# Performance work log

Hardware: AMD Instinct MI355X
Metric: run time of the kernel (lower is better)

Reference implementation:

```python
import jax, jax.numpy as jnp
import numpy as np

MARGIN = 1.0

def setup_inputs() -> dict:
    key = jax.random.key(0)
    k1, k2, k3, k4 = jax.random.split(key, 4)
    N, d, P = 8192, 1024, 65536
    embeddings = jax.random.normal(k1, (N, d), dtype=jnp.float32)
    ind_one = jax.random.randint(k2, (P,), 0, N)
    ind_two = jax.random.randint(k3, (P,), 0, N)
    target = jax.random.randint(k4, (P,), 0, 2)
    return {"embeddings": embeddings, "ind_one": ind_one, "ind_two": ind_two, "target": target}

def reference(embeddings, ind_one, ind_two, target):
    # cosine distance matrix: 1 - normalized gram matrix  [N, N]
    emb_norm = embeddings / jnp.linalg.norm(embeddings, axis=1, keepdims=True)
    dist_matrix = 1.0 - jnp.einsum('nd,md->nm', emb_norm, emb_norm)
    dists = dist_matrix[ind_one, ind_two]  # [P]
    t = target.astype(jnp.float32)
    loss = t * dists + (1.0 - t) * jax.nn.relu(MARGIN - dists)
    return jnp.mean(loss)
```

## Files before the change

### kernel.cpp

```cpp
#include <hip/hip_runtime.h>

#define N_EMB 8192
#define DIM   1024
#define NPAIR 65536
#define MARGIN 1.0f

__global__ __launch_bounds__(256) void norms_kernel(const float* __restrict__ emb,
                                                    float* __restrict__ rnorm,
                                                    double* __restrict__ acc) {
    const int row  = blockIdx.x;
    const int tid  = threadIdx.x;
    const float4 v = reinterpret_cast<const float4*>(emb + (size_t)row * DIM)[tid];
    float s = v.x * v.x + v.y * v.y + v.z * v.z + v.w * v.w;

    #pragma unroll
    for (int off = 32; off > 0; off >>= 1) s += __shfl_xor(s, off);

    __shared__ float part[4];
    const int wave = tid >> 6;
    const int lane = tid & 63;
    if (lane == 0) part[wave] = s;
    __syncthreads();
    if (tid == 0) {
        float tot = part[0] + part[1] + part[2] + part[3];
        rnorm[row] = 1.0f / sqrtf(tot);
        if (row == 0) *acc = 0.0;
    }
}

__global__ __launch_bounds__(256) void pair_kernel(const float* __restrict__ emb,
                                                   const float* __restrict__ rnorm,
                                                   const int* __restrict__ ind1,
                                                   const int* __restrict__ ind2,
                                                   const int* __restrict__ tgt,
                                                   double* __restrict__ acc) {
    const int lane   = threadIdx.x & 63;
    const int wave   = (blockIdx.x * blockDim.x + threadIdx.x) >> 6;
    const int nwaves = (gridDim.x * blockDim.x) >> 6;

    float wsum = 0.0f;

    for (int p = wave; p < NPAIR; p += nwaves) {
        const int a = ind1[p];
        const int b = ind2[p];
        const float4* ra = reinterpret_cast<const float4*>(emb + (size_t)a * DIM);
        const float4* rb = reinterpret_cast<const float4*>(emb + (size_t)b * DIM);

        const float4 a0 = ra[lane];
        const float4 a1 = ra[lane + 64];
        const float4 a2 = ra[lane + 128];
        const float4 a3 = ra[lane + 192];
        const float4 b0 = rb[lane];
        const float4 b1 = rb[lane + 64];
        const float4 b2 = rb[lane + 128];
        const float4 b3 = rb[lane + 192];

        float s = a0.x * b0.x;
        s = fmaf(a0.y, b0.y, s);
        s = fmaf(a0.z, b0.z, s);
        s = fmaf(a0.w, b0.w, s);
        s = fmaf(a1.x, b1.x, s);
        s = fmaf(a1.y, b1.y, s);
        s = fmaf(a1.z, b1.z, s);
        s = fmaf(a1.w, b1.w, s);
        s = fmaf(a2.x, b2.x, s);
        s = fmaf(a2.y, b2.y, s);
        s = fmaf(a2.z, b2.z, s);
        s = fmaf(a2.w, b2.w, s);
        s = fmaf(a3.x, b3.x, s);
        s = fmaf(a3.y, b3.y, s);
        s = fmaf(a3.z, b3.z, s);
        s = fmaf(a3.w, b3.w, s);

        #pragma unroll
        for (int off = 32; off > 0; off >>= 1) s += __shfl_xor(s, off);

        const float dist = 1.0f - s * rnorm[a] * rnorm[b];
        const float t    = (float)tgt[p];
        const float loss = t * dist + (1.0f - t) * fmaxf(MARGIN - dist, 0.0f);
        if (lane == 0) wsum += loss;
    }

    __shared__ float part[4];
    if (lane == 0) part[threadIdx.x >> 6] = wsum;
    __syncthreads();
    if (threadIdx.x == 0) {
        const float bs = part[0] + part[1] + part[2] + part[3];
        atomicAdd(acc, (double)bs);
    }
}

__global__ void finalize_kernel(const double* __restrict__ acc, float* __restrict__ out) {
    out[0] = (float)(acc[0] / (double)NPAIR);
}

extern "C" void kernel_launch(void* const* d_in, const int* in_sizes, int n_in,
                              void* d_out, int out_size, void* d_ws, size_t ws_size,
                              hipStream_t stream) {
    const float* emb  = (const float*)d_in[0];
    const int*   ind1 = (const int*)d_in[1];
    const int*   ind2 = (const int*)d_in[2];
    const int*   tgt  = (const int*)d_in[3];
    float*       out  = (float*)d_out;

    float*  rnorm = (float*)d_ws;
    double* acc   = (double*)((char*)d_ws + (size_t)N_EMB * sizeof(float));

    norms_kernel<<<N_EMB, 256, 0, stream>>>(emb, rnorm, acc);

    pair_kernel<<<2048, 256, 0, stream>>>(emb, rnorm, ind1, ind2, tgt, acc);

    finalize_kernel<<<1, 1, 0, stream>>>(acc, out);
}
```

Measured before the change: 145.2 us.

## Gather from pre-normalized fp16 embedding table with fdot2 and fuse finalize

A prep kernel normalizes each embedding row and writes it as fp16 into workspace. The pair kernel then gathers half-size rows and accumulates with packed fp16 dot products, which removes the rnorm lookups and halves the gather traffic. The separate finalize kernel is replaced by a last-block-done counter inside the pair kernel. The cost is an extra 16 MB table write plus fp16 rounding of the inputs, and the fast path only runs if the workspace is large enough.

```diff
diff --git a/kernel.cpp b/kernel.cpp
--- a/kernel.cpp
+++ b/kernel.cpp
@@ -5,35 +5,41 @@
 #define NPAIR 65536
 #define MARGIN 1.0f
 
-__global__ __launch_bounds__(256) void norms_kernel(const float* __restrict__ emb,
-                                                    float* __restrict__ rnorm,
-                                                    double* __restrict__ acc) {
-    const int row  = blockIdx.x;
-    const int tid  = threadIdx.x;
+typedef _Float16 h2 __attribute__((ext_vector_type(2)));
+typedef _Float16 h4 __attribute__((ext_vector_type(4)));
+typedef _Float16 h8 __attribute__((ext_vector_type(8)));
+
+
+__global__ __launch_bounds__(256) void prep16_kernel(const float* __restrict__ emb,
+                                                     _Float16* __restrict__ nemb,
+                                                     double* __restrict__ acc,
+                                                     unsigned int* __restrict__ cnt) {
+    const int row = blockIdx.x;
+    const int tid = threadIdx.x;
     const float4 v = reinterpret_cast<const float4*>(emb + (size_t)row * DIM)[tid];
     float s = v.x * v.x + v.y * v.y + v.z * v.z + v.w * v.w;
-
     #pragma unroll
     for (int off = 32; off > 0; off >>= 1) s += __shfl_xor(s, off);
-
     __shared__ float part[4];
-    const int wave = tid >> 6;
-    const int lane = tid & 63;
-    if (lane == 0) part[wave] = s;
+    if ((tid & 63) == 0) part[tid >> 6] = s;
     __syncthreads();
-    if (tid == 0) {
-        float tot = part[0] + part[1] + part[2] + part[3];
-        rnorm[row] = 1.0f / sqrtf(tot);
-        if (row == 0) *acc = 0.0;
-    }
+    const float rn = 1.0f / sqrtf(part[0] + part[1] + part[2] + part[3]);
+    h4 o;
+    o[0] = (_Float16)(v.x * rn);
+    o[1] = (_Float16)(v.y * rn);
+    o[2] = (_Float16)(v.z * rn);
+    o[3] = (_Float16)(v.w * rn);
+    reinterpret_cast<h4*>(nemb + (size_t)row * DIM)[tid] = o;
+    if (row == 0 && tid == 0) { *acc = 0.0; *cnt = 0u; }
 }
 
-__global__ __launch_bounds__(256) void pair_kernel(const float* __restrict__ emb,
-                                                   const float* __restrict__ rnorm,
-                                                   const int* __restrict__ ind1,
-                                                   const int* __restrict__ ind2,
-                                                   const int* __restrict__ tgt,
-                                                   double* __restrict__ acc) {
+__global__ __launch_bounds__(256) void pair16_kernel(const _Float16* __restrict__ nemb,
+                                                     const int* __restrict__ ind1,
+                                                     const int* __restrict__ ind2,
+                                                     const int* __restrict__ tgt,
+                                                     double* __restrict__ acc,
+                                                     unsigned int* __restrict__ cnt,
+                                                     float* __restrict__ out) {
     const int lane   = threadIdx.x & 63;
     const int wave   = (blockIdx.x * blockDim.x + threadIdx.x) >> 6;
     const int nwaves = (gridDim.x * blockDim.x) >> 6;
@@ -43,9 +49,91 @@
     for (int p = wave; p < NPAIR; p += nwaves) {
         const int a = ind1[p];
         const int b = ind2[p];
+        const h8* ra = reinterpret_cast<const h8*>(nemb + (size_t)a * DIM);
+        const h8* rb = reinterpret_cast<const h8*>(nemb + (size_t)b * DIM);
+
+        const h8 a0 = ra[lane];
+        const h8 a1 = ra[lane + 64];
+        const h8 b0 = rb[lane];
+        const h8 b1 = rb[lane + 64];
+
+        float s = 0.0f;
+#if __has_builtin(__builtin_amdgcn_fdot2)
+        #define FD(va, vb, I) do { h2 xa, xb;                                  \
+            xa[0] = va[2*I]; xa[1] = va[2*I + 1];                              \
+            xb[0] = vb[2*I]; xb[1] = vb[2*I + 1];                              \
+            s = __builtin_amdgcn_fdot2(xa, xb, s, false); } while (0)
+        FD(a0, b0, 0); FD(a0, b0, 1); FD(a0, b0, 2); FD(a0, b0, 3);
+        FD(a1, b1, 0); FD(a1, b1, 1); FD(a1, b1, 2); FD(a1, b1, 3);
+        #undef FD
+#else
+        #pragma unroll
+        for (int i = 0; i < 8; ++i) {
+            s = fmaf((float)a0[i], (float)b0[i], s);
+            s = fmaf((float)a1[i], (float)b1[i], s);
+        }
+#endif
+        #pragma unroll
+        for (int off = 32; off > 0; off >>= 1) s += __shfl_xor(s, off);
+
+        if (lane == 0) {
+            const float dist = 1.0f - s;
+            const float t    = (float)tgt[p];
+            wsum += t * dist + (1.0f - t) * fmaxf(MARGIN - dist, 0.0f);
+        }
+    }
+
+    __shared__ float part[4];
+    if (lane == 0) part[threadIdx.x >> 6] = wsum;
+    __syncthreads();
+    if (threadIdx.x == 0) {
+        atomicAdd(acc, (double)(part[0] + part[1] + part[2] + part[3]));
+        __threadfence();
+        const unsigned int done = atomicAdd(cnt, 1u);
+        if (done == gridDim.x - 1) {
+            const double tot = atomicAdd(acc, 0.0);
+            out[0] = (float)(tot / (double)NPAIR);
+        }
+    }
+}
+
+
+__global__ __launch_bounds__(256) void norms_kernel(const float* __restrict__ emb,
+                                                    float* __restrict__ rnorm,
+                                                    double* __restrict__ acc,
+                                                    unsigned int* __restrict__ cnt) {
+    const int row = blockIdx.x;
+    const int tid = threadIdx.x;
+    const float4 v = reinterpret_cast<const float4*>(emb + (size_t)row * DIM)[tid];
+    float s = v.x * v.x + v.y * v.y + v.z * v.z + v.w * v.w;
+    #pragma unroll
+    for (int off = 32; off > 0; off >>= 1) s += __shfl_xor(s, off);
+    __shared__ float part[4];
+    if ((tid & 63) == 0) part[tid >> 6] = s;
+    __syncthreads();
+    if (tid == 0) {
+        rnorm[row] = 1.0f / sqrtf(part[0] + part[1] + part[2] + part[3]);
+        if (row == 0) { *acc = 0.0; *cnt = 0u; }
+    }
+}
+
+__global__ __launch_bounds__(256) void pair32_kernel(const float* __restrict__ emb,
+                                                     const float* __restrict__ rnorm,
+                                                     const int* __restrict__ ind1,
+                                                     const int* __restrict__ ind2,
+                                                     const int* __restrict__ tgt,
+                                                     double* __restrict__ acc,
+                                                     unsigned int* __restrict__ cnt,
+                                                     float* __restrict__ out) {
+    const int lane   = threadIdx.x & 63;
+    const int wave   = (blockIdx.x * blockDim.x + threadIdx.x) >> 6;
+    const int nwaves = (gridDim.x * blockDim.x) >> 6;
+    float wsum = 0.0f;
+    for (int p = wave; p < NPAIR; p += nwaves) {
+        const int a = ind1[p];
+        const int b = ind2[p];
         const float4* ra = reinterpret_cast<const float4*>(emb + (size_t)a * DIM);
         const float4* rb = reinterpret_cast<const float4*>(emb + (size_t)b * DIM);
-
         const float4 a0 = ra[lane];
         const float4 a1 = ra[lane + 64];
         const float4 a2 = ra[lane + 128];
@@ -54,44 +142,31 @@
         const float4 b1 = rb[lane + 64];
         const float4 b2 = rb[lane + 128];
         const float4 b3 = rb[lane + 192];
-
         float s = a0.x * b0.x;
-        s = fmaf(a0.y, b0.y, s);
-        s = fmaf(a0.z, b0.z, s);
-        s = fmaf(a0.w, b0.w, s);
-        s = fmaf(a1.x, b1.x, s);
-        s = fmaf(a1.y, b1.y, s);
-        s = fmaf(a1.z, b1.z, s);
-        s = fmaf(a1.w, b1.w, s);
-        s = fmaf(a2.x, b2.x, s);
-        s = fmaf(a2.y, b2.y, s);
-        s = fmaf(a2.z, b2.z, s);
-        s = fmaf(a2.w, b2.w, s);
-        s = fmaf(a3.x, b3.x, s);
-        s = fmaf(a3.y, b3.y, s);
-        s = fmaf(a3.z, b3.z, s);
-        s = fmaf(a3.w, b3.w, s);
-
+        s = fmaf(a0.y, b0.y, s); s = fmaf(a0.z, b0.z, s); s = fmaf(a0.w, b0.w, s);
+        s = fmaf(a1.x, b1.x, s); s = fmaf(a1.y, b1.y, s); s = fmaf(a1.z, b1.z, s); s = fmaf(a1.w, b1.w, s);
+        s = fmaf(a2.x, b2.x, s); s = fmaf(a2.y, b2.y, s); s = fmaf(a2.z, b2.z, s); s = fmaf(a2.w, b2.w, s);
+        s = fmaf(a3.x, b3.x, s); s = fmaf(a3.y, b3.y, s); s = fmaf(a3.z, b3.z, s); s = fmaf(a3.w, b3.w, s);
         #pragma unroll
         for (int off = 32; off > 0; off >>= 1) s += __shfl_xor(s, off);
-
-        const float dist = 1.0f - s * rnorm[a] * rnorm[b];
-        const float t    = (float)tgt[p];
-        const float loss = t * dist + (1.0f - t) * fmaxf(MARGIN - dist, 0.0f);
-        if (lane == 0) wsum += loss;
+        if (lane == 0) {
+            const float dist = 1.0f - s * rnorm[a] * rnorm[b];
+            const float t    = (float)tgt[p];
+            wsum += t * dist + (1.0f - t) * fmaxf(MARGIN - dist, 0.0f);
+        }
     }
-
     __shared__ float part[4];
     if (lane == 0) part[threadIdx.x >> 6] = wsum;
     __syncthreads();
     if (threadIdx.x == 0) {
-        const float bs = part[0] + part[1] + part[2] + part[3];
-        atomicAdd(acc, (double)bs);
+        atomicAdd(acc, (double)(part[0] + part[1] + part[2] + part[3]));
+        __threadfence();
+        const unsigned int done = atomicAdd(cnt, 1u);
+        if (done == gridDim.x - 1) {
+            const double tot = atomicAdd(acc, 0.0);
+            out[0] = (float)(tot / (double)NPAIR);
+        }
     }
-}
-
-__global__ void finalize_kernel(const double* __restrict__ acc, float* __restrict__ out) {
-    out[0] = (float)(acc[0] / (double)NPAIR);
 }
 
 extern "C" void kernel_launch(void* const* d_in, const int* in_sizes, int n_in,
@@ -103,12 +178,18 @@
     const int*   tgt  = (const int*)d_in[3];
     float*       out  = (float*)d_out;
 
-    float*  rnorm = (float*)d_ws;
-    double* acc   = (double*)((char*)d_ws + (size_t)N_EMB * sizeof(float));
+    double*       acc = (double*)d_ws;
+    unsigned int* cnt = (unsigned int*)((char*)d_ws + 8);
 
-    norms_kernel<<<N_EMB, 256, 0, stream>>>(emb, rnorm, acc);
+    const size_t table_bytes = (size_t)N_EMB * DIM * sizeof(_Float16);
 
-    pair_kernel<<<2048, 256, 0, stream>>>(emb, rnorm, ind1, ind2, tgt, acc);
-
-    finalize_kernel<<<1, 1, 0, stream>>>(acc, out);
+    if (ws_size >= 64 + table_bytes) {
+        _Float16* nemb = (_Float16*)((char*)d_ws + 64);
+        prep16_kernel<<<N_EMB, 256, 0, stream>>>(emb, nemb, acc, cnt);
+        pair16_kernel<<<2048, 256, 0, stream>>>(nemb, ind1, ind2, tgt, acc, cnt, out);
+    } else {
+        float* rnorm = (float*)((char*)d_ws + 64);
+        norms_kernel<<<N_EMB, 256, 0, stream>>>(emb, rnorm, acc, cnt);
+        pair32_kernel<<<2048, 256, 0, stream>>>(emb, rnorm, ind1, ind2, tgt, acc, cnt, out);
+    }
 }
```

Result: slower. 172.2 us (+18.6%).

## Bucket pairs by first index so each wave reuses its row in registers

Applied to the files above, without the earlier changes.

Pairs are counting-sorted by ind_one through a histogram, a single-block scan and an atomic scatter. Each wave then owns one embedding row, keeps it in registers and walks only its own bucket of partners, so the A-row is never reloaded from memory. The inner loop handles two partners at a time for extra memory-level parallelism, the norm kernel now does four rows per block, and the finalize kernel is folded into a last-block-done counter. This adds three small launches and sorting overhead, and bucket sizes vary between waves, which creates load imbalance.

```diff
diff --git a/kernel.cpp b/kernel.cpp
--- a/kernel.cpp
+++ b/kernel.cpp
@@ -5,93 +5,185 @@
 #define NPAIR 65536
 #define MARGIN 1.0f
 
+#define OFF_BIN   64
+#define OFF_CUR   (OFF_BIN + (N_EMB + 1) * 4 + 4)
+#define OFF_HIST  (OFF_CUR + N_EMB * 4)
+#define OFF_PACK  (OFF_HIST + N_EMB * 4)
+
 __global__ __launch_bounds__(256) void norms_kernel(const float* __restrict__ emb,
                                                     float* __restrict__ rnorm,
-                                                    double* __restrict__ acc) {
-    const int row  = blockIdx.x;
+                                                    int* __restrict__ hist,
+                                                    double* __restrict__ acc,
+                                                    unsigned int* __restrict__ cnt) {
     const int tid  = threadIdx.x;
-    const float4 v = reinterpret_cast<const float4*>(emb + (size_t)row * DIM)[tid];
-    float s = v.x * v.x + v.y * v.y + v.z * v.z + v.w * v.w;
-
+    const int lane = tid & 63;
+    const int row  = blockIdx.x * 4 + (tid >> 6);
+    const float4* r = reinterpret_cast<const float4*>(emb + (size_t)row * DIM);
+    const float4 v0 = r[lane];
+    const float4 v1 = r[lane + 64];
+    const float4 v2 = r[lane + 128];
+    const float4 v3 = r[lane + 192];
+    float s = v0.x*v0.x + v0.y*v0.y + v0.z*v0.z + v0.w*v0.w
+            + v1.x*v1.x + v1.y*v1.y + v1.z*v1.z + v1.w*v1.w
+            + v2.x*v2.x + v2.y*v2.y + v2.z*v2.z + v2.w*v2.w
+            + v3.x*v3.x + v3.y*v3.y + v3.z*v3.z + v3.w*v3.w;
     #pragma unroll
     for (int off = 32; off > 0; off >>= 1) s += __shfl_xor(s, off);
-
-    __shared__ float part[4];
-    const int wave = tid >> 6;
-    const int lane = tid & 63;
-    if (lane == 0) part[wave] = s;
+    if (lane == 0) rnorm[row] = 1.0f / sqrtf(s);
+
+    const int gid = blockIdx.x * 256 + tid;
+    if (gid < N_EMB) hist[gid] = 0;
+    if (gid == N_EMB) { *acc = 0.0; *cnt = 0u; }
+}
+
+__global__ __launch_bounds__(256) void hist_kernel(const int* __restrict__ ind1,
+                                                   int* __restrict__ hist) {
+    const int p = blockIdx.x * 256 + threadIdx.x;
+    if (p < NPAIR) atomicAdd(&hist[ind1[p]], 1);
+}
+
+__global__ __launch_bounds__(256) void scan_kernel(const int* __restrict__ hist,
+                                                   int* __restrict__ bin_start,
+                                                   int* __restrict__ cursor) {
+    const int t = threadIdx.x;
+    int loc[32];
+    int run = 0;
+    #pragma unroll
+    for (int j = 0; j < 32; ++j) { loc[j] = run; run += hist[t * 32 + j]; }
+
+    __shared__ int ps[256];
+    ps[t] = run;
     __syncthreads();
-    if (tid == 0) {
-        float tot = part[0] + part[1] + part[2] + part[3];
-        rnorm[row] = 1.0f / sqrtf(tot);
-        if (row == 0) *acc = 0.0;
-    }
-}
-
-__global__ __launch_bounds__(256) void pair_kernel(const float* __restrict__ emb,
-                                                   const float* __restrict__ rnorm,
-                                                   const int* __restrict__ ind1,
-                                                   const int* __restrict__ ind2,
-                                                   const int* __restrict__ tgt,
-                                                   double* __restrict__ acc) {
-    const int lane   = threadIdx.x & 63;
-    const int wave   = (blockIdx.x * blockDim.x + threadIdx.x) >> 6;
-    const int nwaves = (gridDim.x * blockDim.x) >> 6;
+    for (int d = 1; d < 256; d <<= 1) {
+        const int v = (t >= d) ? ps[t - d] : 0;
+        __syncthreads();
+        ps[t] += v;
+        __syncthreads();
+    }
+    const int excl = ps[t] - run;
+    #pragma unroll
+    for (int j = 0; j < 32; ++j) {
+        const int b = excl + loc[j];
+        bin_start[t * 32 + j] = b;
+        cursor[t * 32 + j]    = b;
+    }
+    if (t == 255) bin_start[N_EMB] = NPAIR;
+}
+
+__global__ __launch_bounds__(256) void scatter_kernel(const int* __restrict__ ind1,
+                                                      const int* __restrict__ ind2,
+                                                      const int* __restrict__ tgt,
+                                                      int* __restrict__ cursor,
+                                                      int* __restrict__ packed) {
+    const int p = blockIdx.x * 256 + threadIdx.x;
+    if (p < NPAIR) {
+        const int a   = ind1[p];
+        const int pos = atomicAdd(&cursor[a], 1);
+        packed[pos] = (ind2[p] << 1) | (tgt[p] & 1);
+    }
+}
+
+__global__ __launch_bounds__(256, 8) void pair_kernel(const float* __restrict__ emb,
+                                                      const float* __restrict__ rnorm,
+                                                      const int* __restrict__ bin_start,
+                                                      const int* __restrict__ packed,
+                                                      double* __restrict__ acc,
+                                                      unsigned int* __restrict__ cnt,
+                                                      float* __restrict__ out) {
+    const int lane = threadIdx.x & 63;
+    const int w    = (blockIdx.x * blockDim.x + threadIdx.x) >> 6;
+
+    const int start = bin_start[w];
+    const int end   = bin_start[w + 1];
+
+    const float4* ra = reinterpret_cast<const float4*>(emb + (size_t)w * DIM);
+    const float4 a0 = ra[lane];
+    const float4 a1 = ra[lane + 64];
+    const float4 a2 = ra[lane + 128];
+    const float4 a3 = ra[lane + 192];
+    const float rna = rnorm[w];
+
+    #define DOTA(S, B0, B1, B2, B3) do {                                      \
+        S = a0.x*B0.x;                                                         \
+        S = fmaf(a0.y,B0.y,S); S = fmaf(a0.z,B0.z,S); S = fmaf(a0.w,B0.w,S);   \
+        S = fmaf(a1.x,B1.x,S); S = fmaf(a1.y,B1.y,S); S = fmaf(a1.z,B1.z,S);   \
+        S = fmaf(a1.w,B1.w,S);                                                 \
+        S = fmaf(a2.x,B2.x,S); S = fmaf(a2.y,B2.y,S); S = fmaf(a2.z,B2.z,S);   \
+        S = fmaf(a2.w,B2.w,S);                                                 \
+        S = fmaf(a3.x,B3.x,S); S = fmaf(a3.y,B3.y,S); S = fmaf(a3.z,B3.z,S);   \
+        S = fmaf(a3.w,B3.w,S);                                                 \
+    } while (0)
 
     float wsum = 0.0f;
-
-    for (int p = wave; p < NPAIR; p += nwaves) {
-        const int a = ind1[p];
-        const int b = ind2[p];
-        const float4* ra = reinterpret_cast<const float4*>(emb + (size_t)a * DIM);
-        const float4* rb = reinterpret_cast<const float4*>(emb + (size_t)b * DIM);
-
-        const float4 a0 = ra[lane];
-        const float4 a1 = ra[lane + 64];
-        const float4 a2 = ra[lane + 128];
-        const float4 a3 = ra[lane + 192];
+    int i = start;
+
+    for (; i + 1 < end; i += 2) {
+        const int pk0 = packed[i];
+        const int pk1 = packed[i + 1];
+        const int b0i = pk0 >> 1;
+        const int b1i = pk1 >> 1;
+        const float4* rb0 = reinterpret_cast<const float4*>(emb + (size_t)b0i * DIM);
+        const float4* rb1 = reinterpret_cast<const float4*>(emb + (size_t)b1i * DIM);
+        const float4 b00 = rb0[lane];
+        const float4 b01 = rb0[lane + 64];
+        const float4 b02 = rb0[lane + 128];
+        const float4 b03 = rb0[lane + 192];
+        const float4 b10 = rb1[lane];
+        const float4 b11 = rb1[lane + 64];
+        const float4 b12 = rb1[lane + 128];
+        const float4 b13 = rb1[lane + 192];
+
+        float s0, s1;
+        DOTA(s0, b00, b01, b02, b03);
+        DOTA(s1, b10, b11, b12, b13);
+
+        #pragma unroll
+        for (int off = 32; off > 0; off >>= 1) {
+            s0 += __shfl_xor(s0, off);
+            s1 += __shfl_xor(s1, off);
+        }
+
+        if (lane == 0) {
+            const float d0 = 1.0f - s0 * rna * rnorm[b0i];
+            const float t0 = (float)(pk0 & 1);
+            wsum += t0 * d0 + (1.0f - t0) * fmaxf(MARGIN - d0, 0.0f);
+            const float d1 = 1.0f - s1 * rna * rnorm[b1i];
+            const float t1 = (float)(pk1 & 1);
+            wsum += t1 * d1 + (1.0f - t1) * fmaxf(MARGIN - d1, 0.0f);
+        }
+    }
+    if (i < end) {
+        const int pk = packed[i];
+        const int bi = pk >> 1;
+        const float4* rb = reinterpret_cast<const float4*>(emb + (size_t)bi * DIM);
         const float4 b0 = rb[lane];
         const float4 b1 = rb[lane + 64];
         const float4 b2 = rb[lane + 128];
         const float4 b3 = rb[lane + 192];
-
-        float s = a0.x * b0.x;
-        s = fmaf(a0.y, b0.y, s);
-        s = fmaf(a0.z, b0.z, s);
-        s = fmaf(a0.w, b0.w, s);
-        s = fmaf(a1.x, b1.x, s);
-        s = fmaf(a1.y, b1.y, s);
-        s = fmaf(a1.z, b1.z, s);
-        s = fmaf(a1.w, b1.w, s);
-        s = fmaf(a2.x, b2.x, s);
-        s = fmaf(a2.y, b2.y, s);
-        s = fmaf(a2.z, b2.z, s);
-        s = fmaf(a2.w, b2.w, s);
-        s = fmaf(a3.x, b3.x, s);
-        s = fmaf(a3.y, b3.y, s);
-        s = fmaf(a3.z, b3.z, s);
-        s = fmaf(a3.w, b3.w, s);
-
+        float s;
+        DOTA(s, b0, b1, b2, b3);
         #pragma unroll
         for (int off = 32; off > 0; off >>= 1) s += __shfl_xor(s, off);
-
-        const float dist = 1.0f - s * rnorm[a] * rnorm[b];
-        const float t    = (float)tgt[p];
-        const float loss = t * dist + (1.0f - t) * fmaxf(MARGIN - dist, 0.0f);
-        if (lane == 0) wsum += loss;
-    }
+        if (lane == 0) {
+            const float d = 1.0f - s * rna * rnorm[bi];
+            const float t = (float)(pk & 1);
+            wsum += t * d + (1.0f - t) * fmaxf(MARGIN - d, 0.0f);
+        }
+    }
+    #undef DOTA
 
     __shared__ float part[4];
     if (lane == 0) part[threadIdx.x >> 6] = wsum;
     __syncthreads();
     if (threadIdx.x == 0) {
-        const float bs = part[0] + part[1] + part[2] + part[3];
-        atomicAdd(acc, (double)bs);
-    }
-}
-
-__global__ void finalize_kernel(const double* __restrict__ acc, float* __restrict__ out) {
-    out[0] = (float)(acc[0] / (double)NPAIR);
+        atomicAdd(acc, (double)(part[0] + part[1] + part[2] + part[3]));
+        __threadfence();
+        const unsigned int done = atomicAdd(cnt, 1u);
+        if (done == gridDim.x - 1) {
+            const double tot = atomicAdd(acc, 0.0);
+            out[0] = (float)(tot / (double)NPAIR);
+        }
+    }
 }
 
 extern "C" void kernel_launch(void* const* d_in, const int* in_sizes, int n_in,
@@ -103,12 +195,18 @@
     const int*   tgt  = (const int*)d_in[3];
     float*       out  = (float*)d_out;
 
-    float*  rnorm = (float*)d_ws;
-    double* acc   = (double*)((char*)d_ws + (size_t)N_EMB * sizeof(float));
-
-    norms_kernel<<<N_EMB, 256, 0, stream>>>(emb, rnorm, acc);
-
-    pair_kernel<<<2048, 256, 0, stream>>>(emb, rnorm, ind1, ind2, tgt, acc);
-
-    finalize_kernel<<<1, 1, 0, stream>>>(acc, out);
-}
+    char* ws = (char*)d_ws;
+    double*       acc       = (double*)ws;
+    unsigned int* cnt       = (unsigned int*)(ws + 8);
+    int*          bin_start = (int*)(ws + OFF_BIN);
+    int*          cursor    = (int*)(ws + OFF_CUR);
+    int*          hist      = (int*)(ws + OFF_HIST);
+    int*          packed    = (int*)(ws + OFF_PACK);
+    float*        rnorm     = (float*)(ws + OFF_PACK + (size_t)NPAIR * 4);
+
+    norms_kernel<<<N_EMB / 4, 256, 0, stream>>>(emb, rnorm, hist, acc, cnt);
+    hist_kernel<<<NPAIR / 256, 256, 0, stream>>>(ind1, hist);
+    scan_kernel<<<1, 256, 0, stream>>>(hist, bin_start, cursor);
+    scatter_kernel<<<NPAIR / 256, 256, 0, stream>>>(ind1, ind2, tgt, cursor, packed);
+    pair_kernel<<<N_EMB / 4, 256, 0, stream>>>(emb, rnorm, bin_start, packed, acc, cnt, out);
+}
```

Result: slower. 226.6 us (+56.1%).
